# Kernel optimization log

Measured on AMD Instinct MI355X. Metric: run time of the kernel, lower is better.

The kernel has to match this reference:

```python
import jax, jax.numpy as jnp
from jax import lax
import numpy as np

C_IN, C_OUT, G, K, PAD = 64, 128, 4, 3, 1
P = K * K
CG = C_IN // G
N, H, W = 8, 64, 64
LN_EPS = 1e-6
BN_EPS = 1e-5


def setup_inputs() -> dict:
    key = jax.random.key(0)
    ks = jax.random.split(key, 32)
    r = lambda i, shape, s=0.05: jax.random.normal(ks[i], shape, dtype=jnp.float32) * s
    return dict(
        x=jax.random.normal(ks[0], (N, C_IN, H, W), dtype=jnp.float32),
        reflectance=jax.random.uniform(ks[1], (N, 1, H, W), dtype=jnp.float32),
        gain_w1=r(2, (C_IN, C_IN // 4)), gain_b1=r(3, (C_IN // 4,)),
        gain_w2=r(4, (C_IN // 4, C_IN)), gain_b2=r(5, (C_IN,)),
        tap_w=r(6, (C_IN,)), tap_b=r(7, (C_IN,)),
        dw_w=r(8, (K, K, 1, C_IN)), dw_b=r(9, (C_IN,)),
        ln_g=jnp.ones((C_IN,), jnp.float32), ln_b=jnp.zeros((C_IN,), jnp.float32),
        inp_w=r(10, (C_IN, C_IN)), inp_b=r(11, (C_IN,)),
        off_w=r(12, (C_IN, G * P * 2), 0.02), off_b=r(13, (G * P * 2,), 0.02),
        mask_w=r(14, (C_IN, G * P), 0.02), mask_b=r(15, (G * P,), 0.02),
        outp_w=r(16, (C_IN, C_IN)), outp_b=r(17, (C_IN,)),
        conv_w=r(18, (C_IN, C_OUT)), conv_b=r(19, (C_OUT,)),
        bn1_g=jnp.ones((C_IN,), jnp.float32), bn1_b=jnp.zeros((C_IN,), jnp.float32),
        bn1_m=r(20, (C_IN,)),
        bn1_v=jax.random.uniform(ks[21], (C_IN,), minval=0.5, maxval=1.5),
        bn2_g=jnp.ones((C_OUT,), jnp.float32), bn2_b=jnp.zeros((C_OUT,), jnp.float32),
        bn2_m=r(22, (C_OUT,)),
        bn2_v=jax.random.uniform(ks[23], (C_OUT,), minval=0.5, maxval=1.5),
    )


def _bilinear_gather(xg, py, px):
    # xg: (N, Hp, Wp, G, CG); py/px: (N, H, W, G, P) absolute pixel coords
    # replicates F.grid_sample(mode='bilinear', padding_mode='zeros', align_corners=False)
    n_, Hp, Wp = xg.shape[0], xg.shape[1], xg.shape[2]
    y0 = jnp.floor(py)
    x0 = jnp.floor(px)
    wy = py - y0
    wx = px - x0
    nI = jnp.arange(n_).reshape(n_, 1, 1, 1, 1)
    gI = jnp.arange(G).reshape(1, 1, 1, G, 1)
    out = jnp.zeros(py.shape + (CG,), xg.dtype)
    for dy in (0, 1):
        for dx in (0, 1):
            yi = y0 + dy
            xi = x0 + dx
            w = (wy if dy else 1.0 - wy) * (wx if dx else 1.0 - wx)
            valid = (yi >= 0) & (yi < Hp) & (xi >= 0) & (xi < Wp)
            yc = jnp.clip(yi, 0, Hp - 1).astype(jnp.int32)
            xc = jnp.clip(xi, 0, Wp - 1).astype(jnp.int32)
            v = xg[nI, yc, xc, gI]  # (N, H, W, G, P, CG)
            out = out + (w * valid.astype(w.dtype))[..., None] * v
    return out


def reference(x, reflectance, gain_w1, gain_b1, gain_w2, gain_b2, tap_w, tap_b,
              dw_w, dw_b, ln_g, ln_b, inp_w, inp_b, off_w, off_b, mask_w, mask_b,
              outp_w, outp_b, conv_w, conv_b, bn1_g, bn1_b, bn1_m, bn1_v,
              bn2_g, bn2_b, bn2_m, bn2_v):
    n_, c_, h_, w_ = x.shape
    # ---- GainBlock (SE-style): x * sigmoid(mlp(avgpool(x))) + x ----
    pooled = x.mean(axis=(2, 3))                               # (N, C)
    g = jax.nn.relu(pooled @ gain_w1 + gain_b1)
    gain = jax.nn.sigmoid(g @ gain_w2 + gain_b2)               # (N, C)
    x = x * gain[:, :, None, None] + x
    # ---- ReflectiveFeedback: x + relu(conv1x1(reflectance)) ----
    refl = jax.nn.relu(reflectance * tap_w[None, :, None, None] + tap_b[None, :, None, None])
    x = x + refl                                               # (N, C, H, W)
    # ---- DCNv3 (pytorch version, group=4, k=3, pad=1, stride=1) ----
    xh = jnp.transpose(x, (0, 2, 3, 1))                        # NHWC
    xp = xh @ inp_w + inp_b                                    # input_proj
    dw = lax.conv_general_dilated(xh, dw_w, (1, 1), 'SAME',
                                  feature_group_count=c_,
                                  dimension_numbers=('NHWC', 'HWIO', 'NHWC')) + dw_b
    mu = dw.mean(-1, keepdims=True)
    var = dw.var(-1, keepdims=True)
    dw = ln_g * (dw - mu) * lax.rsqrt(var + LN_EPS) + ln_b     # LN channels_last
    dw = jax.nn.gelu(dw, approximate=False)
    offset = (dw @ off_w + off_b).reshape(n_, h_, w_, G, P, 2)
    mask = jax.nn.softmax((dw @ mask_w + mask_b).reshape(n_, h_, w_, G, P), axis=-1)
    # dcnv3_core: pad input, build reference + dilation grids (normalized by padded size)
    xpad = jnp.pad(xp, ((0, 0), (PAD, PAD), (PAD, PAD), (0, 0)))
    Hp, Wp = h_ + 2 * PAD, w_ + 2 * PAD
    ctr = (K - 1) // 2  # = (dilation*(k-1))//2 with dilation=1
    ref_y = (jnp.arange(h_, dtype=jnp.float32) + ctr + 0.5) / Hp
    ref_x = (jnp.arange(w_, dtype=jnp.float32) + ctr + 0.5) / Wp
    kk = jnp.arange(K, dtype=jnp.float32) - ctr                # [-1, 0, 1]
    gx = jnp.repeat(kk, K) / Wp                                # w-outer, h-inner order
    gy = jnp.tile(kk, K) / Hp
    loc_x = (ref_x[None, None, :, None, None] + gx[None, None, None, None, :]
             + offset[..., 0] / Wp)                            # (N,H,W,G,P)
    loc_y = (ref_y[None, :, None, None, None] + gy[None, None, None, None, :]
             + offset[..., 1] / Hp)
    px = loc_x * Wp - 0.5   # align_corners=False pixel coords
    py = loc_y * Hp - 0.5
    xg = xpad.reshape(n_, Hp, Wp, G, CG)
    samp = _bilinear_gather(xg, py, px)                        # (N,H,W,G,P,CG)
    dcn = (samp * mask[..., None]).sum(axis=4).reshape(n_, h_, w_, c_)
    dcn = dcn @ outp_w + outp_b                                # output_proj
    y = jnp.transpose(dcn, (0, 3, 1, 2))                       # back to NCHW
    # ---- bn1 -> relu -> conv1x1 -> bn2 -> relu (eval-mode BN) ----
    y = bn1_g[None, :, None, None] * (y - bn1_m[None, :, None, None]) \
        * lax.rsqrt(bn1_v[None, :, None, None] + BN_EPS) + bn1_b[None, :, None, None]
    y = jax.nn.relu(y)
    y = jnp.einsum('nchw,cd->ndhw', y, conv_w) + conv_b[None, :, None, None]
    y = bn2_g[None, :, None, None] * (y - bn2_m[None, :, None, None]) \
        * lax.rsqrt(bn2_v[None, :, None, None] + BN_EPS) + bn2_b[None, :, None, None]
    return jax.nn.relu(y)
```

## Files before the change

kernel.cpp:

```cpp
#include <hip/hip_runtime.h>
#include <math.h>


__global__ __launch_bounds__(256) void k_pool(const float* x, float* pooled) {
    __shared__ float red[256];
    int b = blockIdx.x;
    int nc = ((b & 7) << 6) | (b >> 3);
    const float4* p4 = reinterpret_cast<const float4*>(x + (size_t)nc * 4096);
    float s = 0.f;
    for (int i = threadIdx.x; i < 1024; i += 256) {
        float4 v = p4[i];
        s += v.x + v.y + v.z + v.w;
    }
    red[threadIdx.x] = s;
    __syncthreads();
    for (int o = 128; o > 0; o >>= 1) {
        if (threadIdx.x < o) red[threadIdx.x] += red[threadIdx.x + o];
        __syncthreads();
    }
    if (threadIdx.x == 0) pooled[nc] = red[0] * (1.f / 4096.f);
}

__global__ __launch_bounds__(256) void k_xsproj(
        const float* x, const float* refl,
        const float* tap_w, const float* tap_b,
        const float* pooled,
        const float* gw1, const float* gb1,
        const float* gw2, const float* gb2,
        const float* inp_w, const float* inp_b,
        float* xs, float* xpad) {
    __shared__ float tile[64 * 17];
    __shared__ float xsrow[16][68];
    __shared__ float hid[16];
    __shared__ float gain[64];
    __shared__ float rrow[16];
    int b = blockIdx.x;
    int n = b & 7, rem = b >> 3;
    int h = rem >> 2, wc = rem & 3, w0 = wc * 16;
    int nh = n * 64 + h;
    int tid = threadIdx.x;

    {
        int c = tid >> 2, wq = (tid & 3) * 4;
        const float4 v = *reinterpret_cast<const float4*>(
            &x[(((size_t)(n * 64 + c)) * 64 + h) * 64 + w0 + wq]);
        tile[c * 17 + wq + 0] = v.x;
        tile[c * 17 + wq + 1] = v.y;
        tile[c * 17 + wq + 2] = v.z;
        tile[c * 17 + wq + 3] = v.w;
    }
    if (tid < 16) rrow[tid] = refl[n * 4096 + h * 64 + w0 + tid];
    if (tid >= 64 && tid < 80) {
        int j = tid - 64;
        float s = gb1[j];
        for (int c = 0; c < 64; ++c) s += pooled[n * 64 + c] * gw1[c * 16 + j];
        hid[j] = fmaxf(s, 0.f);
    }
    __syncthreads();

    if (tid < 64) {
        float s = gb2[tid];
        #pragma unroll
        for (int j = 0; j < 16; ++j) s += hid[j] * gw2[j * 64 + tid];
        gain[tid] = 1.f + 1.f / (1.f + __expf(-s));
    }
    __syncthreads();

    {
        int c = tid & 63, wbq = tid >> 6;
        float gv = gain[c], tw = tap_w[c], tb = tap_b[c];
        #pragma unroll
        for (int k = 0; k < 4; ++k) {
            int w = wbq + k * 4;
            float r = fmaxf(rrow[w] * tw + tb, 0.f);
            float v = tile[c * 17 + w] * gv + r;
            xsrow[w][c] = v;
            xs[(((size_t)nh) * 64 + w0 + w) * 64 + c] = v;
        }
    }
    __syncthreads();

    {
        int co = tid & 63, wg = tid >> 6;
        float acc[4];
        float bv = inp_b[co];
        #pragma unroll
        for (int i = 0; i < 4; ++i) acc[i] = bv;
        for (int c4 = 0; c4 < 64; c4 += 4) {
            float q0 = inp_w[(c4 + 0) * 64 + co];
            float q1 = inp_w[(c4 + 1) * 64 + co];
            float q2 = inp_w[(c4 + 2) * 64 + co];
            float q3 = inp_w[(c4 + 3) * 64 + co];
            #pragma unroll
            for (int i = 0; i < 4; ++i) {
                float4 d = *reinterpret_cast<const float4*>(&xsrow[wg * 4 + i][c4]);
                acc[i] += d.x * q0 + d.y * q1 + d.z * q2 + d.w * q3;
            }
        }
        const size_t rowb = (((size_t)n * 66) + (h + 1)) * 66;
        #pragma unroll
        for (int i = 0; i < 4; ++i) {
            int w = wg * 4 + i;
            xpad[(rowb + (w0 + w + 1)) * 64 + co] = acc[i];
        }
        if (wc == 0 && tid < 64) xpad[rowb * 64 + tid] = 0.f;
        if (wc == 3 && tid < 64) xpad[(rowb + 65) * 64 + tid] = 0.f;
        if (h == 0 || h == 63) {
            const size_t rb = (((size_t)n * 66) + (h == 0 ? 0 : 65)) * 66;
            for (int i = tid; i < 1024; i += 256) {
                int q = 1 + w0 + (i >> 6), cc = i & 63;
                xpad[(rb + q) * 64 + cc] = 0.f;
            }
            if (wc == 0 && tid < 64) xpad[rb * 64 + tid] = 0.f;
            if (wc == 3 && tid < 64) xpad[(rb + 65) * 64 + tid] = 0.f;
        }
    }
}

__global__ __launch_bounds__(128) void k_dwsamp(const float* xs, const float* xpad,
                       const float* dw_w, const float* dw_b,
                       const float* ln_g, const float* ln_b,
                       const float* off_w, const float* off_b,
                       const float* mask_w, const float* mask_b,
                       const float* outp_w, const float* outp_b,
                       const float* bn1_g, const float* bn1_b,
                       const float* bn1_m, const float* bn1_v,
                       const float* conv_w, const float* conv_b,
                       const float* bn2_g, const float* bn2_b,
                       const float* bn2_m, const float* bn2_v,
                       float* out) {
    __shared__ float  dwr[8][64];
    __shared__ float  mlog[8][40];
    __shared__ int4   sad[8][36];
    __shared__ float4 swt[8][36];
    __shared__ float  dcnl[8][64];

    int tid = threadIdx.x;
    int lane = tid & 63, wv = tid >> 6;
    int b = blockIdx.x;
    int n = b & 7;
    int pos0 = (b >> 3) * 8 + wv * 4;
    int h = pos0 >> 6, w0 = pos0 & 63;
    int lbase = wv * 4;

    {
        float dwk[9];
        #pragma unroll
        for (int k = 0; k < 9; ++k) dwk[k] = dw_w[k * 64 + lane];
        float s[4];
        float bvv = dw_b[lane];
        #pragma unroll
        for (int p = 0; p < 4; ++p) s[p] = bvv;
        for (int ky = 0; ky < 3; ++ky) {
            int y = h + ky - 1;
            if (y < 0 || y > 63) continue;
            const float* xrow = xs + ((size_t)(n * 64 + y)) * 4096;
            float v[6];
            #pragma unroll
            for (int dx = 0; dx < 6; ++dx) {
                int x2 = w0 - 1 + dx;
                v[dx] = (x2 >= 0 && x2 <= 63) ? xrow[x2 * 64 + lane] : 0.f;
            }
            float k0 = dwk[ky * 3 + 0], k1 = dwk[ky * 3 + 1], k2 = dwk[ky * 3 + 2];
            #pragma unroll
            for (int p = 0; p < 4; ++p)
                s[p] += v[p] * k0 + v[p + 1] * k1 + v[p + 2] * k2;
        }
        float lngv = ln_g[lane], lnbv = ln_b[lane];
        #pragma unroll
        for (int p = 0; p < 4; ++p) {
            float sv = s[p];
            float sum = sv, sq = sv * sv;
            #pragma unroll
            for (int o = 32; o > 0; o >>= 1) {
                sum += __shfl_xor(sum, o, 64);
                sq  += __shfl_xor(sq,  o, 64);
            }
            float mu = sum * (1.f / 64.f);
            float var = sq * (1.f / 64.f) - mu * mu;
            float nrm = (sv - mu) * rsqrtf(var + 1e-6f) * lngv + lnbv;
            dwr[lbase + p][lane] = 0.5f * nrm * (1.f + erff(nrm * 0.70710678118654752f));
        }
    }
    __syncthreads();

    float a0[4], a1[4];
    {
        int jb = lane * 2;
        const float* wptr;
        int stride;
        float b0 = 0.f, b1 = 0.f;
        if (lane < 36)      { wptr = off_w + jb;         stride = 72; b0 = off_b[jb];       b1 = off_b[jb + 1]; }
        else if (lane < 54) { wptr = mask_w + (jb - 72); stride = 36; b0 = mask_b[jb - 72]; b1 = mask_b[jb - 71]; }
        else                { wptr = off_w;              stride = 0; }
        #pragma unroll
        for (int p = 0; p < 4; ++p) { a0[p] = b0; a1[p] = b1; }
        for (int c4 = 0; c4 < 64; c4 += 4) {
            float4 d0 = *reinterpret_cast<const float4*>(&dwr[lbase + 0][c4]);
            float4 d1 = *reinterpret_cast<const float4*>(&dwr[lbase + 1][c4]);
            float4 d2 = *reinterpret_cast<const float4*>(&dwr[lbase + 2][c4]);
            float4 d3 = *reinterpret_cast<const float4*>(&dwr[lbase + 3][c4]);
            float dk0[4] = {d0.x, d0.y, d0.z, d0.w};
            float dk1[4] = {d1.x, d1.y, d1.z, d1.w};
            float dk2[4] = {d2.x, d2.y, d2.z, d2.w};
            float dk3[4] = {d3.x, d3.y, d3.z, d3.w};
            #pragma unroll
            for (int k = 0; k < 4; ++k) {
                float2 w2 = *reinterpret_cast<const float2*>(wptr);
                wptr += stride;
                a0[0] += dk0[k] * w2.x;  a1[0] += dk0[k] * w2.y;
                a0[1] += dk1[k] * w2.x;  a1[1] += dk1[k] * w2.y;
                a0[2] += dk2[k] * w2.x;  a1[2] += dk2[k] * w2.y;
                a0[3] += dk3[k] * w2.x;  a1[3] += dk3[k] * w2.y;
            }
        }
        if (lane >= 36 && lane < 54) {
            int jm = lane * 2 - 72;
            #pragma unroll
            for (int p = 0; p < 4; ++p) {
                mlog[lbase + p][jm]     = a0[p];
                mlog[lbase + p][jm + 1] = a1[p];
            }
        }
    }
    __syncthreads();

    if (lane < 36) {
        int g = lane / 9, pp = lane - g * 9;
        #pragma unroll
        for (int p = 0; p < 4; ++p) {
            int li = lbase + p;
            const float* lrow = &mlog[li][g * 9];
            float m = lrow[0];
            #pragma unroll
            for (int k = 1; k < 9; ++k) m = fmaxf(m, lrow[k]);
            float ssum = 0.f, ek = 0.f;
            #pragma unroll
            for (int k = 0; k < 9; ++k) {
                float e = __expf(lrow[k] - m);
                ssum += e;
                if (k == pp) ek = e;
            }
            float mk = ek / ssum;
            float px = (float)((w0 + p) + (pp / 3)) + a0[p];
            float py = (float)(h + (pp % 3)) + a1[p];
            float x0f = floorf(px), y0f = floorf(py);
            float wx = px - x0f, wy = py - y0f;
            int x0 = (int)x0f, y0 = (int)y0f;
            int x1 = x0 + 1, y1 = y0 + 1;
            int xc0 = min(max(x0, 0), 65), xc1 = min(max(x1, 0), 65);
            int yc0 = min(max(y0, 0), 65), yc1 = min(max(y1, 0), 65);
            float vx0 = (x0 >= 0 && x0 < 66) ? 1.f : 0.f;
            float vx1 = (x1 >= 0 && x1 < 66) ? 1.f : 0.f;
            float vy0 = (y0 >= 0 && y0 < 66) ? 1.f : 0.f;
            float vy1 = (y1 >= 0 && y1 < 66) ? 1.f : 0.f;
            float wx0 = (1.f - wx) * vx0, wx1 = wx * vx1;
            float wy0 = (1.f - wy) * vy0, wy1 = wy * vy1;
            swt[li][lane] = make_float4(mk * wy0 * wx0, mk * wy0 * wx1,
                                        mk * wy1 * wx0, mk * wy1 * wx1);
            sad[li][lane] = make_int4((yc0 * 66 + xc0) * 64, (yc0 * 66 + xc1) * 64,
                                      (yc1 * 66 + xc0) * 64, (yc1 * 66 + xc1) * 64);
        }
    }
    __syncthreads();

    {
        int gb = (lane >> 4) * 9;
        const float* xpn = xpad + (size_t)n * 66 * 66 * 64;
        #pragma unroll
        for (int p = 0; p < 4; ++p) {
            int li = lbase + p;
            float acc = 0.f;
            #pragma unroll
            for (int pp = 0; pp < 9; ++pp) {
                int4   a  = sad[li][gb + pp];
                float4 cw = swt[li][gb + pp];
                acc += cw.x * xpn[a.x + lane] + cw.y * xpn[a.y + lane]
                     + cw.z * xpn[a.z + lane] + cw.w * xpn[a.w + lane];
            }
            dcnl[li][lane] = acc;
        }
    }
    __syncthreads();

    {
        float ob = outp_b[lane];
        float s0 = ob, s1 = ob, s2 = ob, s3 = ob;
        for (int c4 = 0; c4 < 64; c4 += 4) {
            float w0v = outp_w[(c4 + 0) * 64 + lane];
            float w1v = outp_w[(c4 + 1) * 64 + lane];
            float w2v = outp_w[(c4 + 2) * 64 + lane];
            float w3v = outp_w[(c4 + 3) * 64 + lane];
            float4 d0 = *reinterpret_cast<const float4*>(&dcnl[lbase + 0][c4]);
            float4 d1 = *reinterpret_cast<const float4*>(&dcnl[lbase + 1][c4]);
            float4 d2 = *reinterpret_cast<const float4*>(&dcnl[lbase + 2][c4]);
            float4 d3 = *reinterpret_cast<const float4*>(&dcnl[lbase + 3][c4]);
            s0 += d0.x * w0v + d0.y * w1v + d0.z * w2v + d0.w * w3v;
            s1 += d1.x * w0v + d1.y * w1v + d1.z * w2v + d1.w * w3v;
            s2 += d2.x * w0v + d2.y * w1v + d2.z * w2v + d2.w * w3v;
            s3 += d3.x * w0v + d3.y * w1v + d3.z * w2v + d3.w * w3v;
        }
        float sc = bn1_g[lane] * rsqrtf(bn1_v[lane] + 1e-5f);
        float sh = bn1_b[lane] - sc * bn1_m[lane];
        dcnl[lbase + 0][lane] = fmaxf(sc * s0 + sh, 0.f);
        dcnl[lbase + 1][lane] = fmaxf(sc * s1 + sh, 0.f);
        dcnl[lbase + 2][lane] = fmaxf(sc * s2 + sh, 0.f);
        dcnl[lbase + 3][lane] = fmaxf(sc * s3 + sh, 0.f);
    }

    {
        float accA[4], accB[4];
        #pragma unroll
        for (int p = 0; p < 4; ++p) { accA[p] = 0.f; accB[p] = 0.f; }
        for (int c4 = 0; c4 < 64; c4 += 4) {
            float4 d0 = *reinterpret_cast<const float4*>(&dcnl[lbase + 0][c4]);
            float4 d1 = *reinterpret_cast<const float4*>(&dcnl[lbase + 1][c4]);
            float4 d2 = *reinterpret_cast<const float4*>(&dcnl[lbase + 2][c4]);
            float4 d3 = *reinterpret_cast<const float4*>(&dcnl[lbase + 3][c4]);
            float dk0[4] = {d0.x, d0.y, d0.z, d0.w};
            float dk1[4] = {d1.x, d1.y, d1.z, d1.w};
            float dk2[4] = {d2.x, d2.y, d2.z, d2.w};
            float dk3[4] = {d3.x, d3.y, d3.z, d3.w};
            #pragma unroll
            for (int k = 0; k < 4; ++k) {
                float wa = conv_w[(c4 + k) * 128 + lane];
                float wb = conv_w[(c4 + k) * 128 + 64 + lane];
                accA[0] += dk0[k] * wa;  accB[0] += dk0[k] * wb;
                accA[1] += dk1[k] * wa;  accB[1] += dk1[k] * wb;
                accA[2] += dk2[k] * wa;  accB[2] += dk2[k] * wb;
                accA[3] += dk3[k] * wa;  accB[3] += dk3[k] * wb;
            }
        }
        int dA = lane, dB = lane + 64;
        float scA = bn2_g[dA] * rsqrtf(bn2_v[dA] + 1e-5f);
        float shA = scA * (conv_b[dA] - bn2_m[dA]) + bn2_b[dA];
        float scB = bn2_g[dB] * rsqrtf(bn2_v[dB] + 1e-5f);
        float shB = scB * (conv_b[dB] - bn2_m[dB]) + bn2_b[dB];
        float4 rA, rB;
        rA.x = fmaxf(scA * accA[0] + shA, 0.f);
        rA.y = fmaxf(scA * accA[1] + shA, 0.f);
        rA.z = fmaxf(scA * accA[2] + shA, 0.f);
        rA.w = fmaxf(scA * accA[3] + shA, 0.f);
        rB.x = fmaxf(scB * accB[0] + shB, 0.f);
        rB.y = fmaxf(scB * accB[1] + shB, 0.f);
        rB.z = fmaxf(scB * accB[2] + shB, 0.f);
        rB.w = fmaxf(scB * accB[3] + shB, 0.f);
        size_t oA = (((size_t)(n * 128 + dA)) * 64 + h) * 64 + w0;
        size_t oB = (((size_t)(n * 128 + dB)) * 64 + h) * 64 + w0;
        *reinterpret_cast<float4*>(out + oA) = rA;
        *reinterpret_cast<float4*>(out + oB) = rB;
    }
}

extern "C" void kernel_launch(void* const* d_in, const int* in_sizes, int n_in,
                              void* d_out, int out_size, void* d_ws, size_t ws_size,
                              hipStream_t stream) {
    const float* x      = (const float*)d_in[0];
    const float* refl   = (const float*)d_in[1];
    const float* gw1    = (const float*)d_in[2];
    const float* gb1    = (const float*)d_in[3];
    const float* gw2    = (const float*)d_in[4];
    const float* gb2    = (const float*)d_in[5];
    const float* tap_w  = (const float*)d_in[6];
    const float* tap_b  = (const float*)d_in[7];
    const float* dw_w   = (const float*)d_in[8];
    const float* dw_b   = (const float*)d_in[9];
    const float* ln_g   = (const float*)d_in[10];
    const float* ln_b   = (const float*)d_in[11];
    const float* inp_w  = (const float*)d_in[12];
    const float* inp_b  = (const float*)d_in[13];
    const float* off_w  = (const float*)d_in[14];
    const float* off_b  = (const float*)d_in[15];
    const float* mask_w = (const float*)d_in[16];
    const float* mask_b = (const float*)d_in[17];
    const float* outp_w = (const float*)d_in[18];
    const float* outp_b = (const float*)d_in[19];
    const float* conv_w = (const float*)d_in[20];
    const float* conv_b = (const float*)d_in[21];
    const float* bn1_g  = (const float*)d_in[22];
    const float* bn1_b  = (const float*)d_in[23];
    const float* bn1_m  = (const float*)d_in[24];
    const float* bn1_v  = (const float*)d_in[25];
    const float* bn2_g  = (const float*)d_in[26];
    const float* bn2_b  = (const float*)d_in[27];
    const float* bn2_m  = (const float*)d_in[28];
    const float* bn2_v  = (const float*)d_in[29];

    float* ws     = (float*)d_ws;
    float* pooled = ws;
    float* xs     = ws + 512;
    float* xpad   = xs + 2097152;

    k_pool<<<512, 256, 0, stream>>>(x, pooled);
    k_xsproj<<<2048, 256, 0, stream>>>(x, refl, tap_w, tap_b, pooled,
                                       gw1, gb1, gw2, gb2, inp_w, inp_b, xs, xpad);
    k_dwsamp<<<4096, 128, 0, stream>>>(xs, xpad, dw_w, dw_b, ln_g, ln_b,
                                       off_w, off_b, mask_w, mask_b,
                                       outp_w, outp_b, bn1_g, bn1_b, bn1_m, bn1_v,
                                       conv_w, conv_b, bn2_g, bn2_b, bn2_m, bn2_v,
                                       (float*)d_out);
}
```

Baseline: 191.8 us.

## Hoist gain MLP to its own kernel and make stages wave-local without barriers

Moves the per-batch gain MLP (pooled -> hidden -> sigmoid gain) out of k_xsproj into a tiny k_gain kernel, so the 2048 projection blocks no longer each recompute it. k_xsproj drops to 128 threads, so each wavefront owns 8 pixels end to end. The row staging and the input-projection GEMM are therefore wave-local and need no barrier between them. The same reasoning removes several __syncthreads in k_dwsamp, where each wave handles its own rows in shared memory. This adds an extra kernel launch and relies on implicit wavefront-synchronous LDS ordering, which the compiler does not guarantee.

```diff
diff --git a/kernel.cpp b/kernel.cpp
--- a/kernel.cpp
+++ b/kernel.cpp
@@ -21,18 +21,35 @@
     if (threadIdx.x == 0) pooled[nc] = red[0] * (1.f / 4096.f);
 }
 
-__global__ __launch_bounds__(256) void k_xsproj(
+__global__ __launch_bounds__(128) void k_gain(const float* pooled,
+                       const float* gw1, const float* gb1,
+                       const float* gw2, const float* gb2,
+                       float* gain1p) {
+    __shared__ float hid[16];
+    int n = blockIdx.x;
+    int tid = threadIdx.x;
+    if (tid < 16) {
+        float s = gb1[tid];
+        for (int c = 0; c < 64; ++c) s += pooled[n * 64 + c] * gw1[c * 16 + tid];
+        hid[tid] = fmaxf(s, 0.f);
+    }
+    __syncthreads();
+    if (tid < 64) {
+        float s = gb2[tid];
+        #pragma unroll
+        for (int j = 0; j < 16; ++j) s += hid[j] * gw2[j * 64 + tid];
+        gain1p[n * 64 + tid] = 1.f + 1.f / (1.f + __expf(-s));
+    }
+}
+
+__global__ __launch_bounds__(128) void k_xsproj(
         const float* x, const float* refl,
         const float* tap_w, const float* tap_b,
-        const float* pooled,
-        const float* gw1, const float* gb1,
-        const float* gw2, const float* gb2,
+        const float* gain1p,
         const float* inp_w, const float* inp_b,
         float* xs, float* xpad) {
     __shared__ float tile[64 * 17];
     __shared__ float xsrow[16][68];
-    __shared__ float hid[16];
-    __shared__ float gain[64];
     __shared__ float rrow[16];
     int b = blockIdx.x;
     int n = b & 7, rem = b >> 3;
@@ -41,73 +58,59 @@
     int tid = threadIdx.x;
 
     {
-        int c = tid >> 2, wq = (tid & 3) * 4;
-        const float4 v = *reinterpret_cast<const float4*>(
-            &x[(((size_t)(n * 64 + c)) * 64 + h) * 64 + w0 + wq]);
-        tile[c * 17 + wq + 0] = v.x;
-        tile[c * 17 + wq + 1] = v.y;
-        tile[c * 17 + wq + 2] = v.z;
-        tile[c * 17 + wq + 3] = v.w;
+        int c = tid >> 1, wq = (tid & 1) * 8;
+        const float* src = &x[(((size_t)(n * 64 + c)) * 64 + h) * 64 + w0 + wq];
+        float4 v0 = *reinterpret_cast<const float4*>(src);
+        float4 v1 = *reinterpret_cast<const float4*>(src + 4);
+        tile[c * 17 + wq + 0] = v0.x; tile[c * 17 + wq + 1] = v0.y;
+        tile[c * 17 + wq + 2] = v0.z; tile[c * 17 + wq + 3] = v0.w;
+        tile[c * 17 + wq + 4] = v1.x; tile[c * 17 + wq + 5] = v1.y;
+        tile[c * 17 + wq + 6] = v1.z; tile[c * 17 + wq + 7] = v1.w;
     }
     if (tid < 16) rrow[tid] = refl[n * 4096 + h * 64 + w0 + tid];
-    if (tid >= 64 && tid < 80) {
-        int j = tid - 64;
-        float s = gb1[j];
-        for (int c = 0; c < 64; ++c) s += pooled[n * 64 + c] * gw1[c * 16 + j];
-        hid[j] = fmaxf(s, 0.f);
-    }
     __syncthreads();
 
-    if (tid < 64) {
-        float s = gb2[tid];
-        #pragma unroll
-        for (int j = 0; j < 16; ++j) s += hid[j] * gw2[j * 64 + tid];
-        gain[tid] = 1.f + 1.f / (1.f + __expf(-s));
-    }
-    __syncthreads();
-
-    {
-        int c = tid & 63, wbq = tid >> 6;
-        float gv = gain[c], tw = tap_w[c], tb = tap_b[c];
-        #pragma unroll
-        for (int k = 0; k < 4; ++k) {
-            int w = wbq + k * 4;
+    {
+        int c = tid & 63, wg = tid >> 6;
+        float gv = gain1p[n * 64 + c], tw = tap_w[c], tb = tap_b[c];
+        #pragma unroll
+        for (int k = 0; k < 8; ++k) {
+            int w = wg * 8 + k;
             float r = fmaxf(rrow[w] * tw + tb, 0.f);
             float v = tile[c * 17 + w] * gv + r;
             xsrow[w][c] = v;
             xs[(((size_t)nh) * 64 + w0 + w) * 64 + c] = v;
         }
     }
-    __syncthreads();
 
     {
         int co = tid & 63, wg = tid >> 6;
-        float acc[4];
+        float acc[8];
         float bv = inp_b[co];
         #pragma unroll
-        for (int i = 0; i < 4; ++i) acc[i] = bv;
+        for (int i = 0; i < 8; ++i) acc[i] = bv;
         for (int c4 = 0; c4 < 64; c4 += 4) {
             float q0 = inp_w[(c4 + 0) * 64 + co];
             float q1 = inp_w[(c4 + 1) * 64 + co];
             float q2 = inp_w[(c4 + 2) * 64 + co];
             float q3 = inp_w[(c4 + 3) * 64 + co];
             #pragma unroll
-            for (int i = 0; i < 4; ++i) {
-                float4 d = *reinterpret_cast<const float4*>(&xsrow[wg * 4 + i][c4]);
+            for (int i = 0; i < 8; ++i) {
+                float4 d = *reinterpret_cast<const float4*>(&xsrow[wg * 8 + i][c4]);
                 acc[i] += d.x * q0 + d.y * q1 + d.z * q2 + d.w * q3;
             }
         }
         const size_t rowb = (((size_t)n * 66) + (h + 1)) * 66;
         #pragma unroll
-        for (int i = 0; i < 4; ++i) {
-            int w = wg * 4 + i;
+        for (int i = 0; i < 8; ++i) {
+            int w = wg * 8 + i;
             xpad[(rowb + (w0 + w + 1)) * 64 + co] = acc[i];
         }
         if (wc == 0 && tid < 64) xpad[rowb * 64 + tid] = 0.f;
         if (wc == 3 && tid < 64) xpad[(rowb + 65) * 64 + tid] = 0.f;
         if (h == 0 || h == 63) {
             const size_t rb = (((size_t)n * 66) + (h == 0 ? 0 : 65)) * 66;
-            for (int i = tid; i < 1024; i += 256) {
+            for (int i = tid; i < 1024; i += 128) {
                 int q = 1 + w0 + (i >> 6), cc = i & 63;
                 xpad[(rb + q) * 64 + cc] = 0.f;
             }
@@ -182,7 +185,6 @@
             dwr[lbase + p][lane] = 0.5f * nrm * (1.f + erff(nrm * 0.70710678118654752f));
         }
     }
-    __syncthreads();
 
     float a0[4], a1[4];
     {
@@ -223,7 +225,6 @@
             }
         }
     }
-    __syncthreads();
 
     if (lane < 36) {
         int g = lane / 9, pp = lane - g * 9;
@@ -262,7 +263,6 @@
                                       (yc1 * 66 + xc0) * 64, (yc1 * 66 + xc1) * 64);
         }
     }
-    __syncthreads();
 
     {
         int gb = (lane >> 4) * 9;
@@ -281,7 +281,6 @@
             dcnl[li][lane] = acc;
         }
     }
-    __syncthreads();
 
     {
         float ob = outp_b[lane];
@@ -388,12 +387,14 @@
 
     float* ws     = (float*)d_ws;
     float* pooled = ws;
-    float* xs     = ws + 512;
+    float* gain1p = ws + 512;
+    float* xs     = ws + 1024;
     float* xpad   = xs + 2097152;
 
     k_pool<<<512, 256, 0, stream>>>(x, pooled);
-    k_xsproj<<<2048, 256, 0, stream>>>(x, refl, tap_w, tap_b, pooled,
-                                       gw1, gb1, gw2, gb2, inp_w, inp_b, xs, xpad);
+    k_gain<<<8, 128, 0, stream>>>(pooled, gw1, gb1, gw2, gb2, gain1p);
+    k_xsproj<<<2048, 128, 0, stream>>>(x, refl, tap_w, tap_b, gain1p,
+                                       inp_w, inp_b, xs, xpad);
     k_dwsamp<<<4096, 128, 0, stream>>>(xs, xpad, dw_w, dw_b, ln_g, ln_b,
                                        off_w, off_b, mask_w, mask_b,
                                        outp_w, outp_b, bn1_g, bn1_b, bn1_m, bn1_v,
```

New measurement: 198.1 us. +3.3%, slower.
